# Kernel tuning notes

Measured on AMD Instinct MI355X. Metric: run time of the kernel, lower is better.

Reference implementation:

```python
import jax, jax.numpy as jnp
import numpy as np

S, D_MODEL, D_RNN = 256, 512, 512  # module's broadcasting requires d_rnn == d_model


def setup_inputs() -> dict:
    key = jax.random.key(0)
    k1, k2, k3, k4 = jax.random.split(key, 4)
    x = jax.random.normal(k1, (S, D_MODEL), dtype=jnp.float32)
    state = jnp.zeros((D_RNN, D_MODEL), dtype=jnp.float32)
    # equinox nn.Linear default init: U[-1/sqrt(in), 1/sqrt(in)] for weight and bias
    lim = 1.0 / np.sqrt(D_MODEL)
    W1 = jax.random.uniform(k2, (2 * D_RNN, D_MODEL), minval=-lim, maxval=lim, dtype=jnp.float32)
    b1 = jax.random.uniform(k3, (2 * D_RNN,), minval=-lim, maxval=lim, dtype=jnp.float32)
    # Lambda init exactly as in source: inv_sigmoid(p) = log(1/(1-p)), bounds ** (1/8)
    inv_sig = lambda p: np.log(1.0 / (1.0 - p))
    lower = float(np.power(inv_sig(0.9), 1.0 / 8.0))
    upper = float(np.power(inv_sig(0.999), 1.0 / 8.0))
    Lambda = jax.random.uniform(k4, (D_MODEL,), minval=lower, maxval=upper, dtype=jnp.float32)
    return {"x": x, "state": state, "W1": W1, "b1": b1, "Lambda": Lambda}


def reference(x, state, W1, b1, Lambda):
    # lin1 applied per timestep: (S, d_model) @ (d_model, 2*d_rnn)
    z = jax.nn.sigmoid(x @ W1.T + b1)              # (S, 2*d_rnn)
    inp, rec = jnp.split(z, 2, axis=-1)            # each (S, d_rnn)
    # recurrence gate a_t in (0,1): exp(-8 * softplus(Lambda) * rec)
    a = jnp.exp(-8.0 * jax.nn.softplus(Lambda)[None, :] * rec)  # (S, d_rnn)
    # gated input: outer product per step -> (S, d_rnn, d_model)
    gated_x = jnp.einsum('is,is,id->isd', jnp.sqrt(1.0 - a * a), inp, x)

    def step(h, xs):
        g, at = xs
        h = at[:, None] * h + g                    # (d_rnn, d_model)
        return h, h

    state, y = jax.lax.scan(step, state, (gated_x, a))
    return (y, state)
```

## Files before the change

### kernel.cpp

```cpp
#include <hip/hip_runtime.h>
#include <hip/hip_bf16.h>

#define S_LEN 256
#define DM    512
#define DR    512

typedef float f4 __attribute__((ext_vector_type(4)));
typedef float f2 __attribute__((ext_vector_type(2)));


__global__ __launch_bounds__(256) void k_transpose_x(const float* __restrict__ x,
                                                     float* __restrict__ xT) {
    __shared__ float tile[32][33];
    const int k0 = blockIdx.x * 32;
    const int t0 = blockIdx.y * 32;
    const int lx = threadIdx.x & 31;
    const int ly = threadIdx.x >> 5;
#pragma unroll
    for (int i = 0; i < 32; i += 8)
        tile[ly + i][lx] = x[(t0 + ly + i) * DM + k0 + lx];
    __syncthreads();
#pragma unroll
    for (int i = 0; i < 32; i += 8)
        xT[(k0 + ly + i) * S_LEN + t0 + lx] = tile[lx][ly + i];
}

__global__ __launch_bounds__(256) void k_gemm_act(const float* __restrict__ xT,
                                                  const float* __restrict__ W1,
                                                  const float* __restrict__ b1,
                                                  const float* __restrict__ Lam,
                                                  f2* __restrict__ acT) {
    const int g  = blockIdx.x;
    const int t  = threadIdx.x;
    const int r0 = 2 * g;

    float acc0 = 0.f, acc1 = 0.f, acc2 = 0.f, acc3 = 0.f;
    const float* __restrict__ xb = xT + t;
    const float* __restrict__ w0 = W1 + (r0)       * DM;
    const float* __restrict__ w1 = W1 + (r0 + 1)   * DM;
    const float* __restrict__ w2 = W1 + (512 + r0) * DM;
    const float* __restrict__ w3 = W1 + (513 + r0) * DM;

#pragma unroll 8
    for (int k = 0; k < DM; ++k) {
        const float xv = xb[k * S_LEN];
        acc0 = fmaf(xv, w0[k], acc0);
        acc1 = fmaf(xv, w1[k], acc1);
        acc2 = fmaf(xv, w2[k], acc2);
        acc3 = fmaf(xv, w3[k], acc3);
    }

#pragma unroll
    for (int j = 0; j < 2; ++j) {
        const float pre_i = (j ? acc1 : acc0) + b1[r0 + j];
        const float pre_r = (j ? acc3 : acc2) + b1[512 + r0 + j];
        const float inp = 1.f / (1.f + expf(-pre_i));
        const float rec = 1.f / (1.f + expf(-pre_r));
        const float sp  = log1pf(expf(Lam[r0 + j]));
        const float a   = expf(-8.f * sp * rec);
        const float c   = sqrtf(fmaxf(1.f - a * a, 0.f)) * inp;
        f2 ac; ac.x = a; ac.y = c;
        acT[(r0 + j) * S_LEN + t] = ac;
    }
}

__global__ __launch_bounds__(256) void k_rec(const float* __restrict__ x,
                                             const float* __restrict__ state0,
                                             const f2* __restrict__ acT,
                                             f4* __restrict__ out4) {
    const int bx   = blockIdx.x;
    const int tid  = threadIdx.x;
    const int half = tid >> 7;
    const int s    = bx * 2 + half;
    const int dq   = tid & 127;

    __shared__ f2 ac_l[2][S_LEN];
    f2* lf = &ac_l[0][0];
    lf[tid]       = acT[bx * 2 * S_LEN + tid];
    lf[tid + 256] = acT[bx * 2 * S_LEN + tid + 256];
    __syncthreads();

    const f4* __restrict__ st4 = reinterpret_cast<const f4*>(state0);
    f4 h = st4[s * 128 + dq];

    const f4* __restrict__ x4 = reinterpret_cast<const f4*>(x);
    f4 xv = x4[dq];

#pragma unroll 4
    for (int t = 0; t < S_LEN; ++t) {
        f4 xn;
        if (t + 1 < S_LEN) xn = x4[(t + 1) * 128 + dq];
        else xn = (f4)0.f;

        const f2 ac = ac_l[half][t];
        const float at = ac.x, ct = ac.y;
        h.x = fmaf(at, h.x, ct * xv.x);
        h.y = fmaf(at, h.y, ct * xv.y);
        h.z = fmaf(at, h.z, ct * xv.z);
        h.w = fmaf(at, h.w, ct * xv.w);

        __builtin_nontemporal_store(h, &out4[(t * DR + s) * 128 + dq]);
        xv = xn;
    }
    out4[(S_LEN * DR) * 128 + s * 128 + dq] = h;
}

extern "C" void kernel_launch(void* const* d_in, const int* in_sizes, int n_in,
                              void* d_out, int out_size, void* d_ws, size_t ws_size,
                              hipStream_t stream) {
    const float* x      = (const float*)d_in[0];
    const float* state0 = (const float*)d_in[1];
    const float* W1     = (const float*)d_in[2];
    const float* b1     = (const float*)d_in[3];
    const float* Lam    = (const float*)d_in[4];

    float* ws  = (float*)d_ws;
    float* xT  = ws;
    f2*    acT = (f2*)(ws + 131072);

    f4* out4 = (f4*)d_out;

    k_transpose_x<<<dim3(16, 8), 256, 0, stream>>>(x, xT);
    k_gemm_act<<<dim3(256), 256, 0, stream>>>(xT, W1, b1, Lam, acT);
    k_rec<<<dim3(256), 256, 0, stream>>>(x, state0, acT, out4);
}
```

Baseline: 74.48 us.

## Split linear recurrence into chunked scan with carry, combine, and replay passes

```diff
diff --git a/kernel.cpp b/kernel.cpp
--- a/kernel.cpp
+++ b/kernel.cpp
@@ -4,6 +4,8 @@
 #define S_LEN 256
 #define DM    512
 #define DR    512
+#define NC    8
+#define TC    32
 
 typedef float f4 __attribute__((ext_vector_type(4)));
 typedef float f2 __attribute__((ext_vector_type(2)));
@@ -32,28 +34,26 @@
                                                   f2* __restrict__ acT) {
     const int g  = blockIdx.x;
     const int t  = threadIdx.x;
-    const int r0 = 2 * g;
+    const int r0 = 4 * g;
 
-    float acc0 = 0.f, acc1 = 0.f, acc2 = 0.f, acc3 = 0.f;
+    float ai[4] = {0.f, 0.f, 0.f, 0.f};
+    float ar[4] = {0.f, 0.f, 0.f, 0.f};
     const float* __restrict__ xb = xT + t;
-    const float* __restrict__ w0 = W1 + (r0)       * DM;
-    const float* __restrict__ w1 = W1 + (r0 + 1)   * DM;
-    const float* __restrict__ w2 = W1 + (512 + r0) * DM;
-    const float* __restrict__ w3 = W1 + (513 + r0) * DM;
 
 #pragma unroll 8
     for (int k = 0; k < DM; ++k) {
         const float xv = xb[k * S_LEN];
-        acc0 = fmaf(xv, w0[k], acc0);
-        acc1 = fmaf(xv, w1[k], acc1);
-        acc2 = fmaf(xv, w2[k], acc2);
-        acc3 = fmaf(xv, w3[k], acc3);
+#pragma unroll
+        for (int j = 0; j < 4; ++j) {
+            ai[j] = fmaf(xv, W1[(r0 + j) * DM + k], ai[j]);
+            ar[j] = fmaf(xv, W1[(512 + r0 + j) * DM + k], ar[j]);
+        }
     }
 
 #pragma unroll
-    for (int j = 0; j < 2; ++j) {
-        const float pre_i = (j ? acc1 : acc0) + b1[r0 + j];
-        const float pre_r = (j ? acc3 : acc2) + b1[512 + r0 + j];
+    for (int j = 0; j < 4; ++j) {
+        const float pre_i = ai[j] + b1[r0 + j];
+        const float pre_r = ar[j] + b1[512 + r0 + j];
         const float inp = 1.f / (1.f + expf(-pre_i));
         const float rec = 1.f / (1.f + expf(-pre_r));
         const float sp  = log1pf(expf(Lam[r0 + j]));
@@ -64,45 +64,105 @@
     }
 }
 
-__global__ __launch_bounds__(256) void k_rec(const float* __restrict__ x,
-                                             const float* __restrict__ state0,
-                                             const f2* __restrict__ acT,
-                                             f4* __restrict__ out4) {
-    const int bx   = blockIdx.x;
+__global__ __launch_bounds__(256) void k_carry(const float* __restrict__ x,
+                                               const f2* __restrict__ acT,
+                                               f4* __restrict__ hp,
+                                               float* __restrict__ P) {
+    const int c    = blockIdx.x >> 8;
+    const int g    = blockIdx.x & 255;
     const int tid  = threadIdx.x;
     const int half = tid >> 7;
-    const int s    = bx * 2 + half;
+    const int s    = 2 * g + half;
     const int dq   = tid & 127;
 
-    __shared__ f2 ac_l[2][S_LEN];
-    f2* lf = &ac_l[0][0];
-    lf[tid]       = acT[bx * 2 * S_LEN + tid];
-    lf[tid + 256] = acT[bx * 2 * S_LEN + tid + 256];
+    __shared__ f2 ac_l[2][TC];
+    if (tid < 64) {
+        const int h2 = tid >> 5, tt = tid & 31;
+        ac_l[h2][tt] = acT[(2 * g + h2) * S_LEN + c * TC + tt];
+    }
     __syncthreads();
 
-    const f4* __restrict__ st4 = reinterpret_cast<const f4*>(state0);
-    f4 h = st4[s * 128 + dq];
+    const f4* __restrict__ x4 = reinterpret_cast<const f4*>(x);
+    f4 h = (f4)0.f;
+    float p = 1.f;
 
-    const f4* __restrict__ x4 = reinterpret_cast<const f4*>(x);
-    f4 xv = x4[dq];
-
-#pragma unroll 4
-    for (int t = 0; t < S_LEN; ++t) {
-        f4 xn;
-        if (t + 1 < S_LEN) xn = x4[(t + 1) * 128 + dq];
-        else xn = (f4)0.f;
-
+#pragma unroll
+    for (int t = 0; t < TC; ++t) {
+        const f4 xv = x4[(c * TC + t) * 128 + dq];
         const f2 ac = ac_l[half][t];
         const float at = ac.x, ct = ac.y;
         h.x = fmaf(at, h.x, ct * xv.x);
         h.y = fmaf(at, h.y, ct * xv.y);
         h.z = fmaf(at, h.z, ct * xv.z);
         h.w = fmaf(at, h.w, ct * xv.w);
+        p *= at;
+    }
 
-        __builtin_nontemporal_store(h, &out4[(t * DR + s) * 128 + dq]);
-        xv = xn;
+    hp[(c * DR + s) * 128 + dq] = h;
+    if (dq == 0) P[c * DR + s] = p;
+}
+
+__global__ __launch_bounds__(256) void k_combine(const float* __restrict__ state0,
+                                                 f4* __restrict__ hp,
+                                                 const float* __restrict__ P,
+                                                 f4* __restrict__ out4) {
+    const int gg = blockIdx.x * 256 + threadIdx.x;
+    const int s  = gg >> 7;
+    const int dq = gg & 127;
+
+    const f4* __restrict__ st4 = reinterpret_cast<const f4*>(state0);
+    f4 h = st4[s * 128 + dq];
+
+#pragma unroll
+    for (int c = 0; c < NC; ++c) {
+        const f4 carry = hp[(c * DR + s) * 128 + dq];
+        hp[(c * DR + s) * 128 + dq] = h;
+        const float pc = P[c * DR + s];
+        h.x = fmaf(pc, h.x, carry.x);
+        h.y = fmaf(pc, h.y, carry.y);
+        h.z = fmaf(pc, h.z, carry.z);
+        h.w = fmaf(pc, h.w, carry.w);
     }
     out4[(S_LEN * DR) * 128 + s * 128 + dq] = h;
+}
+
+__global__ __launch_bounds__(256) void k_rec_y(const float* __restrict__ x,
+                                               const f4* __restrict__ hin,
+                                               const f2* __restrict__ acT,
+                                               f4* __restrict__ out4) {
+    const int c    = blockIdx.x >> 8;
+    const int g    = blockIdx.x & 255;
+    const int tid  = threadIdx.x;
+    const int half = tid >> 7;
+    const int s    = 2 * g + half;
+    const int dq   = tid & 127;
+
+    __shared__ f2 ac_l[2][TC];
+    if (tid < 64) {
+        const int h2 = tid >> 5, tt = tid & 31;
+        ac_l[h2][tt] = acT[(2 * g + h2) * S_LEN + c * TC + tt];
+    }
+
+    const f4* __restrict__ x4 = reinterpret_cast<const f4*>(x);
+    f4 h = hin[(c * DR + s) * 128 + dq];
+
+    f4 xbuf[TC];
+#pragma unroll
+    for (int t = 0; t < TC; ++t)
+        xbuf[t] = x4[(c * TC + t) * 128 + dq];
+
+    __syncthreads();
+
+#pragma unroll
+    for (int t = 0; t < TC; ++t) {
+        const f2 ac = ac_l[half][t];
+        const float at = ac.x, ct = ac.y;
+        h.x = fmaf(at, h.x, ct * xbuf[t].x);
+        h.y = fmaf(at, h.y, ct * xbuf[t].y);
+        h.z = fmaf(at, h.z, ct * xbuf[t].z);
+        h.w = fmaf(at, h.w, ct * xbuf[t].w);
+        __builtin_nontemporal_store(h, &out4[((c * TC + t) * DR + s) * 128 + dq]);
+    }
 }
 
 extern "C" void kernel_launch(void* const* d_in, const int* in_sizes, int n_in,
@@ -117,10 +177,14 @@
     float* ws  = (float*)d_ws;
     float* xT  = ws;
     f2*    acT = (f2*)(ws + 131072);
+    f4*    hp  = (f4*)(ws + 393216);
+    float* P   = ws + 2490368;
 
     f4* out4 = (f4*)d_out;
 
     k_transpose_x<<<dim3(16, 8), 256, 0, stream>>>(x, xT);
-    k_gemm_act<<<dim3(256), 256, 0, stream>>>(xT, W1, b1, Lam, acT);
-    k_rec<<<dim3(256), 256, 0, stream>>>(x, state0, acT, out4);
+    k_gemm_act<<<dim3(128), 256, 0, stream>>>(xT, W1, b1, Lam, acT);
+    k_carry<<<dim3(NC * 256), 256, 0, stream>>>(x, acT, hp, P);
+    k_combine<<<dim3(256), 256, 0, stream>>>(state0, hp, P, out4);
+    k_rec_y<<<dim3(NC * 256), 256, 0, stream>>>(x, hp, acT, out4);
 }
```

After: 105.7 us. +42.0%, slower.

## Stage x through double-buffered LDS in recurrence kernel; widen GEMM rows per block

Applied to the files above, without the earlier changes.

```diff
diff --git a/kernel.cpp b/kernel.cpp
--- a/kernel.cpp
+++ b/kernel.cpp
@@ -4,6 +4,8 @@
 #define S_LEN 256
 #define DM    512
 #define DR    512
+#define SECT  8
+#define NSEC  (S_LEN / SECT)
 
 typedef float f4 __attribute__((ext_vector_type(4)));
 typedef float f2 __attribute__((ext_vector_type(2)));
@@ -32,28 +34,26 @@
                                                   f2* __restrict__ acT) {
     const int g  = blockIdx.x;
     const int t  = threadIdx.x;
-    const int r0 = 2 * g;
+    const int r0 = 4 * g;
 
-    float acc0 = 0.f, acc1 = 0.f, acc2 = 0.f, acc3 = 0.f;
+    float ai[4] = {0.f, 0.f, 0.f, 0.f};
+    float ar[4] = {0.f, 0.f, 0.f, 0.f};
     const float* __restrict__ xb = xT + t;
-    const float* __restrict__ w0 = W1 + (r0)       * DM;
-    const float* __restrict__ w1 = W1 + (r0 + 1)   * DM;
-    const float* __restrict__ w2 = W1 + (512 + r0) * DM;
-    const float* __restrict__ w3 = W1 + (513 + r0) * DM;
 
 #pragma unroll 8
     for (int k = 0; k < DM; ++k) {
         const float xv = xb[k * S_LEN];
-        acc0 = fmaf(xv, w0[k], acc0);
-        acc1 = fmaf(xv, w1[k], acc1);
-        acc2 = fmaf(xv, w2[k], acc2);
-        acc3 = fmaf(xv, w3[k], acc3);
+#pragma unroll
+        for (int j = 0; j < 4; ++j) {
+            ai[j] = fmaf(xv, W1[(r0 + j) * DM + k], ai[j]);
+            ar[j] = fmaf(xv, W1[(512 + r0 + j) * DM + k], ar[j]);
+        }
     }
 
 #pragma unroll
-    for (int j = 0; j < 2; ++j) {
-        const float pre_i = (j ? acc1 : acc0) + b1[r0 + j];
-        const float pre_r = (j ? acc3 : acc2) + b1[512 + r0 + j];
+    for (int j = 0; j < 4; ++j) {
+        const float pre_i = ai[j] + b1[r0 + j];
+        const float pre_r = ar[j] + b1[512 + r0 + j];
         const float inp = 1.f / (1.f + expf(-pre_i));
         const float rec = 1.f / (1.f + expf(-pre_r));
         const float sp  = log1pf(expf(Lam[r0 + j]));
@@ -70,38 +70,68 @@
                                              f4* __restrict__ out4) {
     const int bx   = blockIdx.x;
     const int tid  = threadIdx.x;
-    const int half = tid >> 7;
-    const int s    = bx * 2 + half;
-    const int dq   = tid & 127;
+    const int sloc = tid >> 7;
+    const int lane = tid & 63;
+    const int dh   = (tid >> 6) & 1;
+    const int dq   = dh * 64 + lane;
+    const int s    = bx * 2 + sloc;
 
+    __shared__ f4 xbuf[2][SECT][128];
     __shared__ f2 ac_l[2][S_LEN];
-    f2* lf = &ac_l[0][0];
-    lf[tid]       = acT[bx * 2 * S_LEN + tid];
-    lf[tid + 256] = acT[bx * 2 * S_LEN + tid + 256];
-    __syncthreads();
 
+    const f4* __restrict__ x4  = reinterpret_cast<const f4*>(x);
     const f4* __restrict__ st4 = reinterpret_cast<const f4*>(state0);
+
+#pragma unroll
+    for (int i = 0; i < 2; ++i) {
+        const int idx = i * 256 + tid;
+        const int sl = idx >> 8, tt = idx & 255;
+        ac_l[sl][tt] = acT[(bx * 2 + sl) * S_LEN + tt];
+    }
+
     f4 h = st4[s * 128 + dq];
 
-    const f4* __restrict__ x4 = reinterpret_cast<const f4*>(x);
-    f4 xv = x4[dq];
+    f4 xr[4];
+#pragma unroll
+    for (int i = 0; i < 4; ++i) {
+        const int idx = i * 256 + tid;
+        const int tl = idx >> 7, dql = idx & 127;
+        xr[i] = x4[tl * 128 + dql];
+    }
 
-#pragma unroll 4
-    for (int t = 0; t < S_LEN; ++t) {
-        f4 xn;
-        if (t + 1 < S_LEN) xn = x4[(t + 1) * 128 + dq];
-        else xn = (f4)0.f;
+    for (int ss = 0; ss < NSEC; ++ss) {
+        const int buf = ss & 1;
+#pragma unroll
+        for (int i = 0; i < 4; ++i) {
+            const int idx = i * 256 + tid;
+            const int tl = idx >> 7, dql = idx & 127;
+            xbuf[buf][tl][dql] = xr[i];
+        }
+        asm volatile("s_waitcnt lgkmcnt(0)" ::: "memory");
+        __builtin_amdgcn_s_barrier();
 
-        const f2 ac = ac_l[half][t];
-        const float at = ac.x, ct = ac.y;
-        h.x = fmaf(at, h.x, ct * xv.x);
-        h.y = fmaf(at, h.y, ct * xv.y);
-        h.z = fmaf(at, h.z, ct * xv.z);
-        h.w = fmaf(at, h.w, ct * xv.w);
+        if (ss + 1 < NSEC) {
+#pragma unroll
+            for (int i = 0; i < 4; ++i) {
+                const int idx = i * 256 + tid;
+                const int tl = idx >> 7, dql = idx & 127;
+                xr[i] = x4[((ss + 1) * SECT + tl) * 128 + dql];
+            }
+        }
 
-        __builtin_nontemporal_store(h, &out4[(t * DR + s) * 128 + dq]);
-        xv = xn;
+        const int t0 = ss * SECT;
+#pragma unroll
+        for (int t = 0; t < SECT; ++t) {
+            const f2 ac = ac_l[sloc][t0 + t];
+            const f4 xv = xbuf[buf][t][dq];
+            h.x = fmaf(ac.x, h.x, ac.y * xv.x);
+            h.y = fmaf(ac.x, h.y, ac.y * xv.y);
+            h.z = fmaf(ac.x, h.z, ac.y * xv.z);
+            h.w = fmaf(ac.x, h.w, ac.y * xv.w);
+            __builtin_nontemporal_store(h, &out4[((t0 + t) * DR + s) * 128 + dq]);
+        }
     }
+
     out4[(S_LEN * DR) * 128 + s * 128 + dq] = h;
 }
 
@@ -121,6 +151,6 @@
     f4* out4 = (f4*)d_out;
 
     k_transpose_x<<<dim3(16, 8), 256, 0, stream>>>(x, xT);
-    k_gemm_act<<<dim3(256), 256, 0, stream>>>(xT, W1, b1, Lam, acT);
+    k_gemm_act<<<dim3(128), 256, 0, stream>>>(xT, W1, b1, Lam, acT);
     k_rec<<<dim3(256), 256, 0, stream>>>(x, state0, acT, out4);
 }
```

Measured after the change: 83.47 us. 12.1% more time.

## Fuse gate GEMM into recurrence kernel with one state row per block

Applied to the files above, without the earlier changes.

```diff
diff --git a/kernel.cpp b/kernel.cpp
--- a/kernel.cpp
+++ b/kernel.cpp
@@ -25,84 +25,66 @@
         xT[(k0 + ly + i) * S_LEN + t0 + lx] = tile[lx][ly + i];
 }
 
-__global__ __launch_bounds__(256) void k_gemm_act(const float* __restrict__ xT,
-                                                  const float* __restrict__ W1,
-                                                  const float* __restrict__ b1,
-                                                  const float* __restrict__ Lam,
-                                                  f2* __restrict__ acT) {
-    const int g  = blockIdx.x;
-    const int t  = threadIdx.x;
-    const int r0 = 2 * g;
+__global__ __launch_bounds__(256) void k_fused(const float* __restrict__ x,
+                                               const float* __restrict__ xT,
+                                               const float* __restrict__ state0,
+                                               const float* __restrict__ W1,
+                                               const float* __restrict__ b1,
+                                               const float* __restrict__ Lam,
+                                               f2* __restrict__ out2) {
+    const int bx  = blockIdx.x;
+    const int s   = (bx & 7) * 64 + (bx >> 3);
+    const int tid = threadIdx.x;
 
-    float acc0 = 0.f, acc1 = 0.f, acc2 = 0.f, acc3 = 0.f;
-    const float* __restrict__ xb = xT + t;
-    const float* __restrict__ w0 = W1 + (r0)       * DM;
-    const float* __restrict__ w1 = W1 + (r0 + 1)   * DM;
-    const float* __restrict__ w2 = W1 + (512 + r0) * DM;
-    const float* __restrict__ w3 = W1 + (513 + r0) * DM;
+    __shared__ f2 ac_l[S_LEN];
+
+    {
+        const int t = tid;
+        float acc_i = 0.f, acc_r = 0.f;
+        const float* __restrict__ xb = xT + t;
+        const float* __restrict__ wi = W1 + s * DM;
+        const float* __restrict__ wr = W1 + (DR + s) * DM;
 
 #pragma unroll 8
-    for (int k = 0; k < DM; ++k) {
-        const float xv = xb[k * S_LEN];
-        acc0 = fmaf(xv, w0[k], acc0);
-        acc1 = fmaf(xv, w1[k], acc1);
-        acc2 = fmaf(xv, w2[k], acc2);
-        acc3 = fmaf(xv, w3[k], acc3);
+        for (int k = 0; k < DM; ++k) {
+            const float xv = xb[k * S_LEN];
+            acc_i = fmaf(xv, wi[k], acc_i);
+            acc_r = fmaf(xv, wr[k], acc_r);
+        }
+
+        const float pre_i = acc_i + b1[s];
+        const float pre_r = acc_r + b1[DR + s];
+        const float inp = 1.f / (1.f + expf(-pre_i));
+        const float rec = 1.f / (1.f + expf(-pre_r));
+        const float sof = log1pf(expf(Lam[s]));
+        const float a   = expf(-8.f * sof * rec);
+        const float c   = sqrtf(fmaxf(1.f - a * a, 0.f)) * inp;
+        f2 ac; ac.x = a; ac.y = c;
+        ac_l[t] = ac;
     }
 
-#pragma unroll
-    for (int j = 0; j < 2; ++j) {
-        const float pre_i = (j ? acc1 : acc0) + b1[r0 + j];
-        const float pre_r = (j ? acc3 : acc2) + b1[512 + r0 + j];
-        const float inp = 1.f / (1.f + expf(-pre_i));
-        const float rec = 1.f / (1.f + expf(-pre_r));
-        const float sp  = log1pf(expf(Lam[r0 + j]));
-        const float a   = expf(-8.f * sp * rec);
-        const float c   = sqrtf(fmaxf(1.f - a * a, 0.f)) * inp;
-        f2 ac; ac.x = a; ac.y = c;
-        acT[(r0 + j) * S_LEN + t] = ac;
-    }
-}
+    const f2* __restrict__ st2 = reinterpret_cast<const f2*>(state0);
+    const f2* __restrict__ x2  = reinterpret_cast<const f2*>(x);
 
-__global__ __launch_bounds__(256) void k_rec(const float* __restrict__ x,
-                                             const float* __restrict__ state0,
-                                             const f2* __restrict__ acT,
-                                             f4* __restrict__ out4) {
-    const int bx   = blockIdx.x;
-    const int tid  = threadIdx.x;
-    const int half = tid >> 7;
-    const int s    = bx * 2 + half;
-    const int dq   = tid & 127;
+    f2 h  = st2[s * 256 + tid];
+    f2 xv = x2[tid];
 
-    __shared__ f2 ac_l[2][S_LEN];
-    f2* lf = &ac_l[0][0];
-    lf[tid]       = acT[bx * 2 * S_LEN + tid];
-    lf[tid + 256] = acT[bx * 2 * S_LEN + tid + 256];
     __syncthreads();
-
-    const f4* __restrict__ st4 = reinterpret_cast<const f4*>(state0);
-    f4 h = st4[s * 128 + dq];
-
-    const f4* __restrict__ x4 = reinterpret_cast<const f4*>(x);
-    f4 xv = x4[dq];
 
 #pragma unroll 4
     for (int t = 0; t < S_LEN; ++t) {
-        f4 xn;
-        if (t + 1 < S_LEN) xn = x4[(t + 1) * 128 + dq];
-        else xn = (f4)0.f;
+        f2 xn;
+        if (t + 1 < S_LEN) xn = x2[(t + 1) * 256 + tid];
+        else xn = (f2)0.f;
 
-        const f2 ac = ac_l[half][t];
-        const float at = ac.x, ct = ac.y;
-        h.x = fmaf(at, h.x, ct * xv.x);
-        h.y = fmaf(at, h.y, ct * xv.y);
-        h.z = fmaf(at, h.z, ct * xv.z);
-        h.w = fmaf(at, h.w, ct * xv.w);
+        const f2 ac = ac_l[t];
+        h.x = fmaf(ac.x, h.x, ac.y * xv.x);
+        h.y = fmaf(ac.x, h.y, ac.y * xv.y);
 
-        __builtin_nontemporal_store(h, &out4[(t * DR + s) * 128 + dq]);
+        __builtin_nontemporal_store(h, &out2[(t * DR + s) * 256 + tid]);
         xv = xn;
     }
-    out4[(S_LEN * DR) * 128 + s * 128 + dq] = h;
+    out2[(S_LEN * DR) * 256 + s * 256 + tid] = h;
 }
 
 extern "C" void kernel_launch(void* const* d_in, const int* in_sizes, int n_in,
@@ -114,13 +96,11 @@
     const float* b1     = (const float*)d_in[3];
     const float* Lam    = (const float*)d_in[4];
 
-    float* ws  = (float*)d_ws;
-    float* xT  = ws;
-    f2*    acT = (f2*)(ws + 131072);
+    float* ws = (float*)d_ws;
+    float* xT = ws;
 
-    f4* out4 = (f4*)d_out;
+    f2* out2 = (f2*)d_out;
 
     k_transpose_x<<<dim3(16, 8), 256, 0, stream>>>(x, xT);
-    k_gemm_act<<<dim3(256), 256, 0, stream>>>(xT, W1, b1, Lam, acT);
-    k_rec<<<dim3(256), 256, 0, stream>>>(x, state0, acT, out4);
+    k_fused<<<dim3(512), 256, 0, stream>>>(x, xT, state0, W1, b1, Lam, out2);
 }
```

Measured after the change: 73.55 us. About the same (-1.3%).
